# Kernel optimization log

Measured on AMD Instinct MI355X. Metric: run time of the kernel, lower is better.

The kernel has to match this reference:

```python
import jax, jax.numpy as jnp
import numpy as np

EMBED_DIM = 1024
NUM_HEADS = 16
HEAD_DIM = EMBED_DIM // NUM_HEADS
SCALING = HEAD_DIM ** -0.5
NEG_FILL = -1e30


def setup_inputs() -> dict:
    key = jax.random.key(0)
    k1, k2, k3 = jax.random.split(key, 3)
    T, B, E = 2048, 4, EMBED_DIM
    query = jax.random.normal(k1, (T, B, E), dtype=jnp.float32)
    key_padding_mask = jnp.zeros((B, T), dtype=bool)  # 1 = padded key
    # xavier_uniform-like init
    lim_in = (6.0 / (3 * E + E)) ** 0.5
    in_proj_weight = jax.random.uniform(k2, (3 * E, E), minval=-lim_in, maxval=lim_in, dtype=jnp.float32)
    in_proj_bias = jnp.zeros((3 * E,), dtype=jnp.float32)
    lim_out = (6.0 / (E + E)) ** 0.5
    out_w = jax.random.uniform(k3, (E, E), minval=-lim_out, maxval=lim_out, dtype=jnp.float32)
    out_b = jnp.zeros((E,), dtype=jnp.float32)
    return {"query": query, "key_padding_mask": key_padding_mask,
            "in_proj_weight": in_proj_weight, "in_proj_bias": in_proj_bias,
            "out_w": out_w, "out_b": out_b}


def reference(query, key_padding_mask, in_proj_weight, in_proj_bias, out_w, out_b):
    T, B, E = query.shape
    H, D = NUM_HEADS, HEAD_DIM
    # fused in-projection (self-attention: qkv from same input)
    qkv = query @ in_proj_weight.T + in_proj_bias  # [T,B,3E]
    q, k, v = jnp.split(qkv, 3, axis=-1)
    q = q * SCALING
    q = q.reshape(T, B, H, D)
    k = k.reshape(T, B, H, D)
    v = v.reshape(T, B, H, D)
    # attention scores [B,H,T,S]
    scores = jnp.einsum('tbhd,sbhd->bhts', q, k)
    scores = jnp.where(key_padding_mask[:, None, None, :], NEG_FILL, scores)
    attn_w = jax.nn.softmax(scores, axis=-1)  # [B,H,T,S]
    # weighted sum of values -> [T,B,E]
    attn = jnp.einsum('bhts,sbhd->tbhd', attn_w, v).reshape(T, B, E)
    attn = attn @ out_w.T + out_b
    attn_w_avg = jnp.sum(attn_w, axis=1) / H  # [B,T,S]
    return attn, attn_w_avg
```

## Files before the change

### kernel.cpp

```cpp
#include <hip/hip_runtime.h>
#include <stdint.h>

#define QSCALE 0.18033688011112042f

typedef unsigned short u16;
typedef unsigned int u32;
typedef __attribute__((ext_vector_type(8))) __bf16 bf16x8;
typedef __attribute__((ext_vector_type(4))) float f32x4;
typedef __attribute__((ext_vector_type(16))) float f32x16;
typedef __attribute__((ext_vector_type(8))) u16 u16x8;
typedef __attribute__((ext_vector_type(4))) u32 u32x4;

__device__ __forceinline__ void gl_lds16(const void* g, void* l) {
  __builtin_amdgcn_global_load_lds(
      (const __attribute__((address_space(1))) void*)g,
      (__attribute__((address_space(3))) void*)l, 16, 0, 0);
}

__device__ __forceinline__ u16 f2bf(float f) {
  unsigned int u = __float_as_uint(f);
  u += 0x7FFFu + ((u >> 16) & 1u);
  return (u16)(u >> 16);
}

extern "C" __global__ __launch_bounds__(256) void cvt_all(
    const float* __restrict__ query, const float* __restrict__ w_in,
    const float* __restrict__ w_out, u16* __restrict__ dst) {
  int i = (blockIdx.x * 256 + threadIdx.x) * 4;
  const float* src;
  int off;
  if (i < 8388608) {
    src = query; off = i;
  } else if (i < 11534336) {
    src = w_in; off = i - 8388608;
  } else {
    src = w_out; off = i - 11534336;
  }
  float4 v = *(const float4*)(src + off);
  ushort4 o;
  o.x = f2bf(v.x); o.y = f2bf(v.y); o.z = f2bf(v.z); o.w = f2bf(v.w);
  *(ushort4*)(dst + i) = o;
}

extern "C" __global__ __launch_bounds__(256) void gemm_qkv(
    const u16* __restrict__ X, const u16* __restrict__ W,
    const float* __restrict__ bias,
    u16* __restrict__ qb, u16* __restrict__ kb, u16* __restrict__ vb) {
  const int tid = threadIdx.x;
  const int w = tid >> 6, lane = tid & 63;
  const int lg = lane >> 4, ll = lane & 15;
  const int wm = w >> 1, wn = w & 1;
  const int row0A = blockIdx.x * 128;
  const int row0B = blockIdx.y * 128;

  __shared__ __align__(16) u16 As[2][128 * 32];
  __shared__ __align__(16) u16 Bs[2][128 * 32];

  f32x4 acc[4][4] = {};

  const int r_st = tid >> 2;
  const int cb_st = (tid & 3) * 16;

#pragma unroll
  for (int it = 0; it < 2; ++it) {
    gl_lds16((const char*)X + ((size_t)(row0A + it * 64 + r_st) * 1024) * 2 + cb_st,
             (char*)&As[0][0] + it * 4096 + w * 1024);
    gl_lds16((const char*)W + ((size_t)(row0B + it * 64 + r_st) * 1024) * 2 + cb_st,
             (char*)&Bs[0][0] + it * 4096 + w * 1024);
  }

  for (int kt = 0; kt < 32; ++kt) {
    const int cur = kt & 1;
    asm volatile("s_waitcnt vmcnt(0)" ::: "memory");
    __syncthreads();
    if (kt + 1 < 32) {
      const int k0 = (kt + 1) * 32;
#pragma unroll
      for (int it = 0; it < 2; ++it) {
        gl_lds16((const char*)X + ((size_t)(row0A + it * 64 + r_st) * 1024 + k0) * 2 + cb_st,
                 (char*)&As[cur ^ 1][0] + it * 4096 + w * 1024);
        gl_lds16((const char*)W + ((size_t)(row0B + it * 64 + r_st) * 1024 + k0) * 2 + cb_st,
                 (char*)&Bs[cur ^ 1][0] + it * 4096 + w * 1024);
      }
    }
    const u16* Ab = &As[cur][0];
    const u16* Bb = &Bs[cur][0];
    const int kc = lg * 8;
    bf16x8 a[4], bfr[4];
#pragma unroll
    for (int i = 0; i < 4; ++i)
      a[i] = *(const bf16x8*)(Ab + (wm * 64 + i * 16 + ll) * 32 + kc);
#pragma unroll
    for (int j = 0; j < 4; ++j)
      bfr[j] = *(const bf16x8*)(Bb + (wn * 64 + j * 16 + ll) * 32 + kc);
#pragma unroll
    for (int i = 0; i < 4; ++i)
#pragma unroll
      for (int j = 0; j < 4; ++j)
        acc[i][j] = __builtin_amdgcn_mfma_f32_16x16x32_bf16(a[i], bfr[j], acc[i][j], 0, 0, 0);
  }

  const int which = row0B >> 10;
  u16* dst = which == 0 ? qb : (which == 1 ? kb : vb);
  const float scl = which == 0 ? QSCALE : 1.0f;
#pragma unroll
  for (int j = 0; j < 4; ++j) {
    const int n = row0B + wn * 64 + j * 16 + ll;
    const float bv = bias[n];
    const int n2 = n & 1023;
    const int hh = n2 >> 6, dd = n2 & 63;
#pragma unroll
    for (int i = 0; i < 4; ++i)
#pragma unroll
      for (int r = 0; r < 4; ++r) {
        const int m = row0A + wm * 64 + i * 16 + lg * 4 + r;
        const int tt = m >> 2, bb = m & 3;
        dst[((size_t)(bb * 16 + hh) * 2048 + tt) * 64 + dd] = f2bf((acc[i][j][r] + bv) * scl);
      }
  }
}

extern "C" __global__ __launch_bounds__(256) void transpose_v(
    const u16* __restrict__ v, u16* __restrict__ vt) {
  const int blk = blockIdx.x;
  const int bh = blk >> 5, tt = blk & 31;
  const int t0 = tt * 64;
  const int tid = threadIdx.x;
  __shared__ __align__(16) u16 tile[64][72];
  const u16* src = v + ((size_t)bh * 2048 + t0) * 64;
#pragma unroll
  for (int it = 0; it < 2; ++it) {
    const int r = it * 32 + (tid >> 3);
    const int c = (tid & 7) * 8;
    *(u16x8*)(&tile[r][c]) = *(const u16x8*)(src + (size_t)r * 64 + c);
  }
  __syncthreads();
  u16* dstb = vt + (size_t)bh * 64 * 2048 + t0;
#pragma unroll
  for (int it = 0; it < 2; ++it) {
    const int d = it * 32 + (tid >> 3);
    const int s = (tid & 7) * 8;
    u16x8 o;
#pragma unroll
    for (int jj = 0; jj < 8; ++jj) o[jj] = tile[s + jj][d];
    *(u16x8*)(dstb + (size_t)d * 2048 + s) = o;
  }
}

extern "C" __global__ __launch_bounds__(256, 3) void flash_fwd(
    const u16* __restrict__ q, const u16* __restrict__ k,
    const u16* __restrict__ vt, const unsigned char* __restrict__ mask,
    u16* __restrict__ attn_pre, float* __restrict__ stat_il) {
  const int lb = ((blockIdx.x & 7) << 7) + (blockIdx.x >> 3);
  const int bh = lb >> 4, tt = lb & 15;
  const int b = bh >> 4, hd = bh & 15;
  const int t0 = tt * 128;
  const int tid = threadIdx.x, w = tid >> 6, lane = tid & 63;
  const int hl = lane >> 5;
  const int l31 = lane & 31;

  __shared__ __align__(16) u16 Ks[3][64 * 64];
  __shared__ __align__(16) u16 Vs[3][64 * 64];
  __shared__ __align__(16) unsigned char Ms[2048];

  const int qrow = t0 + w * 32 + l31;
  const u16* qp = q + ((size_t)bh * 2048 + qrow) * 64 + hl * 8;
  bf16x8 qreg[4];
#pragma unroll
  for (int kg = 0; kg < 4; ++kg) qreg[kg] = *(const bf16x8*)(qp + kg * 16);

  f32x16 po[2] = {};
  float lsum = 0.f;

  const int slot_r = tid >> 3;
  const int slot_c8 = (tid & 7) ^ (slot_r & 7);

#define STAGE3(buf, s0_)                                                       \
  do {                                                                         \
    _Pragma("unroll") for (int it2 = 0; it2 < 2; ++it2) {                      \
      const int rr = it2 * 32 + slot_r;                                        \
      gl_lds16((const char*)k +                                                \
                   (((size_t)bh * 2048 + (s0_) + rr) * 64 + slot_c8 * 8) * 2,  \
               (char*)&Ks[buf][0] + it2 * 4096 + w * 1024);                    \
      gl_lds16((const char*)vt +                                               \
                   (((size_t)bh * 64 + rr) * 2048 + (s0_) + slot_c8 * 8) * 2,  \
               (char*)&Vs[buf][0] + it2 * 4096 + w * 1024);                    \
    }                                                                          \
  } while (0)

  if (w < 2)
    gl_lds16((const char*)mask + b * 2048 + w * 1024 + lane * 16,
             (char*)Ms + w * 1024);
  STAGE3(0, 0);
  STAGE3(1, 64);

  for (int t = 0; t < 32; ++t) {
    if (t < 31) {
      asm volatile("s_waitcnt vmcnt(4)" ::: "memory");
    } else {
      asm volatile("s_waitcnt vmcnt(0)" ::: "memory");
    }
    __builtin_amdgcn_s_barrier();
    if (t + 2 < 32) STAGE3((t + 2) % 3, (t + 2) * 64);

    const int s0 = t * 64;
    const int cur = t % 3;
    const char* Kb = (const char*)&Ks[cur][0];
    const char* Vb = (const char*)&Vs[cur][0];

    u32 mq[8];
#pragma unroll
    for (int kt = 0; kt < 2; ++kt)
#pragma unroll
      for (int j = 0; j < 4; ++j)
        mq[kt * 4 + j] =
            *(const u32*)(Ms + s0 + kt * 32 + j * 8 + hl * 4);
    const u32 anym = mq[0] | mq[1] | mq[2] | mq[3] | mq[4] | mq[5] | mq[6] | mq[7];

#pragma unroll
    for (int kt = 0; kt < 2; ++kt) {
      f32x16 z = {};
      const int key = kt * 32 + l31;
#pragma unroll
      for (int kg = 0; kg < 4; ++kg) {
        const bf16x8 kf = *(const bf16x8*)(
            Kb + key * 128 + ((((kg << 1) | hl) ^ (key & 7)) << 4));
        z = __builtin_amdgcn_mfma_f32_32x32x16_bf16(kf, qreg[kg], z, 0, 0, 0);
      }

      float ps[16];
#pragma unroll
      for (int r = 0; r < 16; ++r) ps[r] = __builtin_amdgcn_exp2f(z[r]);
      if (__any(anym != 0)) {
#pragma unroll
        for (int r = 0; r < 16; ++r)
          if ((mq[kt * 4 + (r >> 2)] >> ((r & 3) * 8)) & 0xFFu) ps[r] = 0.f;
      }
#pragma unroll
      for (int r = 0; r < 16; ++r) lsum += ps[r];

      u32 w8[8];
#pragma unroll
      for (int j = 0; j < 4; ++j) {
        asm("v_cvt_pk_bf16_f32 %0, %1, %2"
            : "=v"(w8[2 * j]) : "v"(ps[4 * j]), "v"(ps[4 * j + 1]));
        asm("v_cvt_pk_bf16_f32 %0, %1, %2"
            : "=v"(w8[2 * j + 1]) : "v"(ps[4 * j + 2]), "v"(ps[4 * j + 3]));
      }

#pragma unroll
      for (int f = 0; f < 2; ++f) {
        u32 d0 = w8[4 * f], d1 = w8[4 * f + 1];
        u32 s0w = w8[4 * f + 2], s1w = w8[4 * f + 3];
        asm volatile("v_permlane32_swap_b32 %0, %1" : "+v"(d0), "+v"(s0w));
        asm volatile("v_permlane32_swap_b32 %0, %1" : "+v"(d1), "+v"(s1w));
        const bf16x8 pa = __builtin_bit_cast(bf16x8, (u32x4){d0, d1, s0w, s1w});
        const int g = kt * 2 + f;
#pragma unroll
        for (int dt = 0; dt < 2; ++dt) {
          const int d = dt * 32 + l31;
          const bf16x8 vf = *(const bf16x8*)(
              Vb + d * 128 + ((((g << 1) | hl) ^ (d & 7)) << 4));
          po[dt] = __builtin_amdgcn_mfma_f32_32x32x16_bf16(pa, vf, po[dt], 0, 0, 0);
        }
      }
    }
  }

  lsum += __shfl_xor(lsum, 32, 64);
  const float linv = 1.0f / lsum;
  if (lane < 32)
    stat_il[(size_t)bh * 2048 + t0 + w * 32 + lane] = linv;

#pragma unroll
  for (int r = 0; r < 16; ++r) {
    const int qi = (r & 3) + 8 * (r >> 2) + 4 * hl;
    const float lv = __shfl(linv, qi, 64);
    const int trow = t0 + w * 32 + qi;
#pragma unroll
    for (int dt = 0; dt < 2; ++dt) {
      const int dd = dt * 32 + l31;
      attn_pre[((size_t)(trow * 4 + b)) * 1024 + hd * 64 + dd] =
          f2bf(po[dt][r] * lv);
    }
  }
#undef STAGE3
}

extern "C" __global__ __launch_bounds__(256, 3) void wavg(
    const u16* __restrict__ q, const u16* __restrict__ k,
    const unsigned char* __restrict__ mask,
    const float* __restrict__ stat_il, float* __restrict__ wout) {
  const int lb = ((blockIdx.x & 7) << 8) + (blockIdx.x >> 3);
  const int b = lb >> 9, tt = (lb >> 5) & 15, st = lb & 31;
  const int t0 = tt * 128, s0 = st * 64;
  const int tid = threadIdx.x, w = tid >> 6, lane = tid & 63;
  const int hl = lane >> 5;
  const int l31 = lane & 31;

  __shared__ __align__(16) u16 Qs[2][128 * 64];
  __shared__ __align__(16) u16 Ks2[2][64 * 64];

  const int slot_r8 = tid >> 3;
  const int slot_c8 = (tid & 7) ^ (slot_r8 & 7);

  u32 mq[8];
#pragma unroll
  for (int kt = 0; kt < 2; ++kt)
#pragma unroll
    for (int j = 0; j < 4; ++j)
      mq[kt * 4 + j] = *(const u32*)(mask + b * 2048 + s0 + kt * 32 + j * 8 + hl * 4);
  const u32 anym = mq[0] | mq[1] | mq[2] | mq[3] | mq[4] | mq[5] | mq[6] | mq[7];
  const bool domask = __any(anym != 0);

#define STAGE_W(buf, hh)                                                       \
  do {                                                                         \
    const size_t qo_ = (size_t)(b * 16 + (hh)) * 2048;                         \
    _Pragma("unroll") for (int i2 = 0; i2 < 4; ++i2) {                         \
      const int rr = i2 * 32 + slot_r8;                                        \
      gl_lds16((const char*)q + ((qo_ + t0 + rr) * 64 + slot_c8 * 8) * 2,      \
               (char*)&Qs[buf][0] + i2 * 4096 + w * 1024);                     \
    }                                                                          \
    _Pragma("unroll") for (int i2 = 0; i2 < 2; ++i2) {                         \
      const int rr = i2 * 32 + slot_r8;                                        \
      gl_lds16((const char*)k + ((qo_ + s0 + rr) * 64 + slot_c8 * 8) * 2,      \
               (char*)&Ks2[buf][0] + i2 * 4096 + w * 1024);                    \
    }                                                                          \
  } while (0)

  STAGE_W(0, 0);
  asm volatile("s_waitcnt vmcnt(0)" ::: "memory");
  __syncthreads();

  float accw[32] = {};
  for (int h = 0; h < 16; ++h) {
    const int cur = h & 1;
    const float ilh =
        stat_il[(size_t)(b * 16 + h) * 2048 + t0 + w * 32 + l31];

    if (h + 1 < 16) STAGE_W(cur ^ 1, h + 1);

    const char* Qb = (const char*)&Qs[cur][0];
    const char* Kb = (const char*)&Ks2[cur][0];

    const int qr = w * 32 + l31;
    bf16x8 qf[4];
#pragma unroll
    for (int kg = 0; kg < 4; ++kg)
      qf[kg] = *(const bf16x8*)(
          Qb + qr * 128 + ((((kg << 1) | hl) ^ (qr & 7)) << 4));

#pragma unroll
    for (int kt = 0; kt < 2; ++kt) {
      f32x16 z = {};
      const int key = kt * 32 + l31;
#pragma unroll
      for (int kg = 0; kg < 4; ++kg) {
        const bf16x8 kf = *(const bf16x8*)(
            Kb + key * 128 + ((((kg << 1) | hl) ^ (key & 7)) << 4));
        z = __builtin_amdgcn_mfma_f32_32x32x16_bf16(kf, qf[kg], z, 0, 0, 0);
      }
      float ps[16];
#pragma unroll
      for (int r = 0; r < 16; ++r) ps[r] = __builtin_amdgcn_exp2f(z[r]);
      if (domask) {
#pragma unroll
        for (int r = 0; r < 16; ++r)
          if ((mq[kt * 4 + (r >> 2)] >> ((r & 3) * 8)) & 0xFFu) ps[r] = 0.f;
      }
#pragma unroll
      for (int r = 0; r < 16; ++r)
        accw[kt * 16 + r] = fmaf(ps[r], ilh, accw[kt * 16 + r]);
    }

    asm volatile("s_waitcnt vmcnt(0)" ::: "memory");
    __syncthreads();
  }

  float* tb = ((float*)&Qs[0][0]) + w * 2048;
#pragma unroll
  for (int kt = 0; kt < 2; ++kt)
#pragma unroll
    for (int j = 0; j < 4; ++j) {
      f32x4 qd;
#pragma unroll
      for (int e = 0; e < 4; ++e) qd[e] = accw[kt * 16 + 4 * j + e] * 0.0625f;
      const int slot = kt * 8 + 2 * j + hl;
      *(f32x4*)(tb + l31 * 64 + ((slot ^ (l31 & 7)) << 2)) = qd;
    }
  __syncthreads();
#pragma unroll
  for (int j2 = 0; j2 < 8; ++j2) {
    const int row = j2 * 4 + (lane >> 4);
    const int slot = lane & 15;
    const f32x4 v = *(const f32x4*)(tb + row * 64 + ((slot ^ (row & 7)) << 2));
    *(f32x4*)(wout + ((size_t)b * 2048 + t0 + w * 32 + row) * 2048 + s0 +
              slot * 4) = v;
  }
#undef STAGE_W
}

extern "C" __global__ __launch_bounds__(256) void gemm_out(
    const u16* __restrict__ A, const u16* __restrict__ W,
    const float* __restrict__ bias, float* __restrict__ out) {
  const int tid = threadIdx.x;
  const int w = tid >> 6, lane = tid & 63;
  const int lg = lane >> 4, ll = lane & 15;
  const int wm = w >> 1, wn = w & 1;
  const int row0A = blockIdx.x * 128;
  const int row0B = blockIdx.y * 128;

  __shared__ __align__(16) u16 As[2][128 * 32];
  __shared__ __align__(16) u16 Bs[2][128 * 32];

  f32x4 acc[4][4] = {};
  const int r_st = tid >> 2;
  const int cb_st = (tid & 3) * 16;

#pragma unroll
  for (int it = 0; it < 2; ++it) {
    gl_lds16((const char*)A + ((size_t)(row0A + it * 64 + r_st) * 1024) * 2 + cb_st,
             (char*)&As[0][0] + it * 4096 + w * 1024);
    gl_lds16((const char*)W + ((size_t)(row0B + it * 64 + r_st) * 1024) * 2 + cb_st,
             (char*)&Bs[0][0] + it * 4096 + w * 1024);
  }

  for (int kt = 0; kt < 32; ++kt) {
    const int cur = kt & 1;
    asm volatile("s_waitcnt vmcnt(0)" ::: "memory");
    __syncthreads();
    if (kt + 1 < 32) {
      const int k0 = (kt + 1) * 32;
#pragma unroll
      for (int it = 0; it < 2; ++it) {
        gl_lds16((const char*)A + ((size_t)(row0A + it * 64 + r_st) * 1024 + k0) * 2 + cb_st,
                 (char*)&As[cur ^ 1][0] + it * 4096 + w * 1024);
        gl_lds16((const char*)W + ((size_t)(row0B + it * 64 + r_st) * 1024 + k0) * 2 + cb_st,
                 (char*)&Bs[cur ^ 1][0] + it * 4096 + w * 1024);
      }
    }
    const u16* Ab = &As[cur][0];
    const u16* Bb = &Bs[cur][0];
    const int kc = lg * 8;
    bf16x8 a[4], bfr[4];
#pragma unroll
    for (int i = 0; i < 4; ++i)
      a[i] = *(const bf16x8*)(Ab + (wm * 64 + i * 16 + ll) * 32 + kc);
#pragma unroll
    for (int j = 0; j < 4; ++j)
      bfr[j] = *(const bf16x8*)(Bb + (wn * 64 + j * 16 + ll) * 32 + kc);
#pragma unroll
    for (int i = 0; i < 4; ++i)
#pragma unroll
      for (int j = 0; j < 4; ++j)
        acc[i][j] = __builtin_amdgcn_mfma_f32_16x16x32_bf16(a[i], bfr[j], acc[i][j], 0, 0, 0);
  }

#pragma unroll
  for (int j = 0; j < 4; ++j) {
    const int n = row0B + wn * 64 + j * 16 + ll;
    const float bv = bias[n];
#pragma unroll
    for (int i = 0; i < 4; ++i)
#pragma unroll
      for (int r = 0; r < 4; ++r) {
        const int m = row0A + wm * 64 + i * 16 + lg * 4 + r;
        out[(size_t)m * 1024 + n] = acc[i][j][r] + bv;
      }
  }
}

extern "C" void kernel_launch(void* const* d_in, const int* in_sizes, int n_in,
                              void* d_out, int out_size, void* d_ws, size_t ws_size,
                              hipStream_t stream) {
  const float* query = (const float*)d_in[0];
  const unsigned char* mask = (const unsigned char*)d_in[1];
  const float* w_in = (const float*)d_in[2];
  const float* b_in = (const float*)d_in[3];
  const float* w_out = (const float*)d_in[4];
  const float* b_out = (const float*)d_in[5];

  float* out0 = (float*)d_out;
  float* outw = out0 + (size_t)8388608;

  char* ws = (char*)d_ws;
  u16* Xbf   = (u16*)(ws + 0);
  u16* Wqkv  = (u16*)(ws + 16777216);
  u16* Woutb = (u16*)(ws + 23068672);
  u16* qb    = (u16*)(ws + 25165824);
  u16* kb    = (u16*)(ws + 41943040);
  u16* vb    = (u16*)(ws + 58720256);
  u16* vtb   = (u16*)(ws + 75497472);
  u16* ap    = (u16*)(ws + 92274688);
  float* sil = (float*)(ws + 109051904);

  cvt_all<<<12288, 256, 0, stream>>>(query, w_in, w_out, Xbf);
  gemm_qkv<<<dim3(64, 24), 256, 0, stream>>>(Xbf, Wqkv, b_in, qb, kb, vb);
  transpose_v<<<2048, 256, 0, stream>>>(vb, vtb);
  flash_fwd<<<1024, 256, 0, stream>>>(qb, kb, vtb, mask, ap, sil);
  wavg<<<2048, 256, 0, stream>>>(qb, kb, mask, sil, outw);
  gemm_out<<<dim3(64, 8), 256, 0, stream>>>(ap, Woutb, b_out, out0);
}
```

Measured before the change: 282.9 us.

## Software-pipeline QK and PV in flash kernel with bitpacked mask

New measurement: 289.9 us. +2.5%, slower.

```diff
diff --git a/kernel.cpp b/kernel.cpp
--- a/kernel.cpp
+++ b/kernel.cpp
@@ -5,6 +5,7 @@
 
 typedef unsigned short u16;
 typedef unsigned int u32;
+typedef unsigned long long u64;
 typedef __attribute__((ext_vector_type(8))) __bf16 bf16x8;
 typedef __attribute__((ext_vector_type(4))) float f32x4;
 typedef __attribute__((ext_vector_type(16))) float f32x16;
@@ -42,6 +43,21 @@
   *(ushort4*)(dst + i) = o;
 }
 
+extern "C" __global__ __launch_bounds__(128) void mask_bits(
+    const unsigned char* __restrict__ mask, u64* __restrict__ mbits) {
+  const int i = threadIdx.x;
+  const unsigned char* p = mask + i * 64;
+  u64 bits = 0;
+#pragma unroll
+  for (int j = 0; j < 8; ++j) {
+    const u64 c = *(const u64*)(p + j * 8);
+#pragma unroll
+    for (int bb = 0; bb < 8; ++bb)
+      if ((c >> (8 * bb)) & 0xFFull) bits |= 1ull << (j * 8 + bb);
+  }
+  mbits[i] = bits;
+}
+
 extern "C" __global__ __launch_bounds__(256) void gemm_qkv(
     const u16* __restrict__ X, const u16* __restrict__ W,
     const float* __restrict__ bias,
@@ -147,9 +163,9 @@
   }
 }
 
-extern "C" __global__ __launch_bounds__(256, 3) void flash_fwd(
+extern "C" __global__ __launch_bounds__(256, 4) void flash_fwd(
     const u16* __restrict__ q, const u16* __restrict__ k,
-    const u16* __restrict__ vt, const unsigned char* __restrict__ mask,
+    const u16* __restrict__ vt, const u64* __restrict__ mbits,
     u16* __restrict__ attn_pre, float* __restrict__ stat_il) {
   const int lb = ((blockIdx.x & 7) << 7) + (blockIdx.x >> 3);
   const int bh = lb >> 4, tt = lb & 15;
@@ -160,8 +176,7 @@
   const int l31 = lane & 31;
 
   __shared__ __align__(16) u16 Ks[3][64 * 64];
-  __shared__ __align__(16) u16 Vs[3][64 * 64];
-  __shared__ __align__(16) unsigned char Ms[2048];
+  __shared__ __align__(16) u16 Vs[2][64 * 64];
 
   const int qrow = t0 + w * 32 + l31;
   const u16* qp = q + ((size_t)bh * 2048 + qrow) * 64 + hl * 8;
@@ -175,96 +190,113 @@
   const int slot_r = tid >> 3;
   const int slot_c8 = (tid & 7) ^ (slot_r & 7);
 
-#define STAGE3(buf, s0_)                                                       \
+#define STAGE_K(s_, buf_)                                                      \
   do {                                                                         \
     _Pragma("unroll") for (int it2 = 0; it2 < 2; ++it2) {                      \
       const int rr = it2 * 32 + slot_r;                                        \
       gl_lds16((const char*)k +                                                \
-                   (((size_t)bh * 2048 + (s0_) + rr) * 64 + slot_c8 * 8) * 2,  \
-               (char*)&Ks[buf][0] + it2 * 4096 + w * 1024);                    \
-      gl_lds16((const char*)vt +                                               \
-                   (((size_t)bh * 64 + rr) * 2048 + (s0_) + slot_c8 * 8) * 2,  \
-               (char*)&Vs[buf][0] + it2 * 4096 + w * 1024);                    \
+                   (((size_t)bh * 2048 + (s_)*64 + rr) * 64 + slot_c8 * 8) * 2,\
+               (char*)&Ks[buf_][0] + it2 * 4096 + w * 1024);                   \
     }                                                                          \
   } while (0)
-
-  if (w < 2)
-    gl_lds16((const char*)mask + b * 2048 + w * 1024 + lane * 16,
-             (char*)Ms + w * 1024);
-  STAGE3(0, 0);
-  STAGE3(1, 64);
-
+#define STAGE_V(s_, buf_)                                                      \
+  do {                                                                         \
+    _Pragma("unroll") for (int it2 = 0; it2 < 2; ++it2) {                      \
+      const int rr = it2 * 32 + slot_r;                                        \
+      gl_lds16((const char*)vt +                                               \
+                   (((size_t)bh * 64 + rr) * 2048 + (s_)*64 + slot_c8 * 8) * 2,\
+               (char*)&Vs[buf_][0] + it2 * 4096 + w * 1024);                   \
+    }                                                                          \
+  } while (0)
+
+  auto QK = [&](int kbuf, int kt, f32x16& z) {
+    const char* Kb = (const char*)&Ks[kbuf][0];
+    f32x16 acc = {};
+    const int key = kt * 32 + l31;
+#pragma unroll
+    for (int kg = 0; kg < 4; ++kg) {
+      const bf16x8 kf = *(const bf16x8*)(
+          Kb + key * 128 + ((((kg << 1) | hl) ^ (key & 7)) << 4));
+      acc = __builtin_amdgcn_mfma_f32_32x32x16_bf16(kf, qreg[kg], acc, 0, 0, 0);
+    }
+    z = acc;
+  };
+
+  auto CONSUME = [&](int vbuf, int kt, const f32x16& z, u32 m32) {
+    u32 w8[8];
+#pragma unroll
+    for (int h2 = 0; h2 < 2; ++h2) {
+      float ps[8];
+#pragma unroll
+      for (int r = 0; r < 8; ++r) {
+        const int ri = h2 * 8 + r;
+        float p = __builtin_amdgcn_exp2f(z[ri]);
+        if (m32) {
+          const int bitpos = (ri & 3) + 8 * (ri >> 2) + 4 * hl;
+          if ((m32 >> bitpos) & 1u) p = 0.f;
+        }
+        lsum += p;
+        ps[r] = p;
+      }
+#pragma unroll
+      for (int j = 0; j < 2; ++j) {
+        asm("v_cvt_pk_bf16_f32 %0, %1, %2"
+            : "=v"(w8[h2 * 4 + 2 * j]) : "v"(ps[4 * j]), "v"(ps[4 * j + 1]));
+        asm("v_cvt_pk_bf16_f32 %0, %1, %2"
+            : "=v"(w8[h2 * 4 + 2 * j + 1]) : "v"(ps[4 * j + 2]), "v"(ps[4 * j + 3]));
+      }
+    }
+    const char* Vb = (const char*)&Vs[vbuf][0];
+#pragma unroll
+    for (int f = 0; f < 2; ++f) {
+      u32 d0 = w8[4 * f], d1 = w8[4 * f + 1];
+      u32 s0w = w8[4 * f + 2], s1w = w8[4 * f + 3];
+      asm volatile("v_permlane32_swap_b32 %0, %1" : "+v"(d0), "+v"(s0w));
+      asm volatile("v_permlane32_swap_b32 %0, %1" : "+v"(d1), "+v"(s1w));
+      const bf16x8 pa = __builtin_bit_cast(bf16x8, (u32x4){d0, d1, s0w, s1w});
+      const int g = kt * 2 + f;
+      __builtin_amdgcn_s_setprio(1);
+#pragma unroll
+      for (int dt = 0; dt < 2; ++dt) {
+        const int d = dt * 32 + l31;
+        const bf16x8 vf = *(const bf16x8*)(
+            Vb + d * 128 + ((((g << 1) | hl) ^ (d & 7)) << 4));
+        po[dt] = __builtin_amdgcn_mfma_f32_32x32x16_bf16(pa, vf, po[dt], 0, 0, 0);
+      }
+      __builtin_amdgcn_s_setprio(0);
+    }
+  };
+
+  STAGE_K(0, 0);
+  STAGE_K(1, 1);
+  STAGE_V(0, 0);
+  asm volatile("s_waitcnt vmcnt(0)" ::: "memory");
+  __builtin_amdgcn_s_barrier();
+
+  f32x16 zA, zB;
+  QK(0, 0, zA);
+
+  int kb0 = 0, kb1 = 1, kb2 = 2;
   for (int t = 0; t < 32; ++t) {
+    const u64 mb = mbits[b * 32 + t];
+    if (t + 2 < 32) STAGE_K(t + 2, kb2);
+    if (t + 1 < 32) STAGE_V(t + 1, (t + 1) & 1);
+
+    __builtin_amdgcn_s_setprio(1);
+    QK(kb0, 1, zB);
+    __builtin_amdgcn_s_setprio(0);
+    CONSUME(t & 1, 0, zA, (u32)mb);
+
     if (t < 31) {
-      asm volatile("s_waitcnt vmcnt(4)" ::: "memory");
-    } else {
-      asm volatile("s_waitcnt vmcnt(0)" ::: "memory");
-    }
+      __builtin_amdgcn_s_setprio(1);
+      QK(kb1, 0, zA);
+      __builtin_amdgcn_s_setprio(0);
+    }
+    CONSUME(t & 1, 1, zB, (u32)(mb >> 32));
+
+    asm volatile("s_waitcnt vmcnt(0)" ::: "memory");
     __builtin_amdgcn_s_barrier();
-    if (t + 2 < 32) STAGE3((t + 2) % 3, (t + 2) * 64);
-
-    const int s0 = t * 64;
-    const int cur = t % 3;
-    const char* Kb = (const char*)&Ks[cur][0];
-    const char* Vb = (const char*)&Vs[cur][0];
-
-    u32 mq[8];
-#pragma unroll
-    for (int kt = 0; kt < 2; ++kt)
-#pragma unroll
-      for (int j = 0; j < 4; ++j)
-        mq[kt * 4 + j] =
-            *(const u32*)(Ms + s0 + kt * 32 + j * 8 + hl * 4);
-    const u32 anym = mq[0] | mq[1] | mq[2] | mq[3] | mq[4] | mq[5] | mq[6] | mq[7];
-
-#pragma unroll
-    for (int kt = 0; kt < 2; ++kt) {
-      f32x16 z = {};
-      const int key = kt * 32 + l31;
-#pragma unroll
-      for (int kg = 0; kg < 4; ++kg) {
-        const bf16x8 kf = *(const bf16x8*)(
-            Kb + key * 128 + ((((kg << 1) | hl) ^ (key & 7)) << 4));
-        z = __builtin_amdgcn_mfma_f32_32x32x16_bf16(kf, qreg[kg], z, 0, 0, 0);
-      }
-
-      float ps[16];
-#pragma unroll
-      for (int r = 0; r < 16; ++r) ps[r] = __builtin_amdgcn_exp2f(z[r]);
-      if (__any(anym != 0)) {
-#pragma unroll
-        for (int r = 0; r < 16; ++r)
-          if ((mq[kt * 4 + (r >> 2)] >> ((r & 3) * 8)) & 0xFFu) ps[r] = 0.f;
-      }
-#pragma unroll
-      for (int r = 0; r < 16; ++r) lsum += ps[r];
-
-      u32 w8[8];
-#pragma unroll
-      for (int j = 0; j < 4; ++j) {
-        asm("v_cvt_pk_bf16_f32 %0, %1, %2"
-            : "=v"(w8[2 * j]) : "v"(ps[4 * j]), "v"(ps[4 * j + 1]));
-        asm("v_cvt_pk_bf16_f32 %0, %1, %2"
-            : "=v"(w8[2 * j + 1]) : "v"(ps[4 * j + 2]), "v"(ps[4 * j + 3]));
-      }
-
-#pragma unroll
-      for (int f = 0; f < 2; ++f) {
-        u32 d0 = w8[4 * f], d1 = w8[4 * f + 1];
-        u32 s0w = w8[4 * f + 2], s1w = w8[4 * f + 3];
-        asm volatile("v_permlane32_swap_b32 %0, %1" : "+v"(d0), "+v"(s0w));
-        asm volatile("v_permlane32_swap_b32 %0, %1" : "+v"(d1), "+v"(s1w));
-        const bf16x8 pa = __builtin_bit_cast(bf16x8, (u32x4){d0, d1, s0w, s1w});
-        const int g = kt * 2 + f;
-#pragma unroll
-        for (int dt = 0; dt < 2; ++dt) {
-          const int d = dt * 32 + l31;
-          const bf16x8 vf = *(const bf16x8*)(
-              Vb + d * 128 + ((((g << 1) | hl) ^ (d & 7)) << 4));
-          po[dt] = __builtin_amdgcn_mfma_f32_32x32x16_bf16(pa, vf, po[dt], 0, 0, 0);
-        }
-      }
-    }
+    const int tmp = kb0; kb0 = kb1; kb1 = kb2; kb2 = tmp;
   }
 
   lsum += __shfl_xor(lsum, 32, 64);
@@ -284,12 +316,13 @@
           f2bf(po[dt][r] * lv);
     }
   }
-#undef STAGE3
+#undef STAGE_K
+#undef STAGE_V
 }
 
 extern "C" __global__ __launch_bounds__(256, 3) void wavg(
     const u16* __restrict__ q, const u16* __restrict__ k,
-    const unsigned char* __restrict__ mask,
+    const u64* __restrict__ mbits,
     const float* __restrict__ stat_il, float* __restrict__ wout) {
   const int lb = ((blockIdx.x & 7) << 8) + (blockIdx.x >> 3);
   const int b = lb >> 9, tt = (lb >> 5) & 15, st = lb & 31;
@@ -304,14 +337,9 @@
   const int slot_r8 = tid >> 3;
   const int slot_c8 = (tid & 7) ^ (slot_r8 & 7);
 
-  u32 mq[8];
-#pragma unroll
-  for (int kt = 0; kt < 2; ++kt)
-#pragma unroll
-    for (int j = 0; j < 4; ++j)
-      mq[kt * 4 + j] = *(const u32*)(mask + b * 2048 + s0 + kt * 32 + j * 8 + hl * 4);
-  const u32 anym = mq[0] | mq[1] | mq[2] | mq[3] | mq[4] | mq[5] | mq[6] | mq[7];
-  const bool domask = __any(anym != 0);
+  const u64 mbw = mbits[b * 32 + st];
+  const u32 m32lo = (u32)mbw, m32hi = (u32)(mbw >> 32);
+  const bool domask = mbw != 0ull;
 
 #define STAGE_W(buf, hh)                                                       \
   do {                                                                         \
@@ -350,27 +378,41 @@
       qf[kg] = *(const bf16x8*)(
           Qb + qr * 128 + ((((kg << 1) | hl) ^ (qr & 7)) << 4));
 
-#pragma unroll
-    for (int kt = 0; kt < 2; ++kt) {
-      f32x16 z = {};
-      const int key = kt * 32 + l31;
-#pragma unroll
-      for (int kg = 0; kg < 4; ++kg) {
-        const bf16x8 kf = *(const bf16x8*)(
-            Kb + key * 128 + ((((kg << 1) | hl) ^ (key & 7)) << 4));
-        z = __builtin_amdgcn_mfma_f32_32x32x16_bf16(kf, qf[kg], z, 0, 0, 0);
-      }
-      float ps[16];
-#pragma unroll
-      for (int r = 0; r < 16; ++r) ps[r] = __builtin_amdgcn_exp2f(z[r]);
+    f32x16 z0 = {}, z1 = {};
+    __builtin_amdgcn_s_setprio(1);
+#pragma unroll
+    for (int kg = 0; kg < 4; ++kg) {
+      const int key = l31;
+      const bf16x8 kf = *(const bf16x8*)(
+          Kb + key * 128 + ((((kg << 1) | hl) ^ (key & 7)) << 4));
+      z0 = __builtin_amdgcn_mfma_f32_32x32x16_bf16(kf, qf[kg], z0, 0, 0, 0);
+    }
+#pragma unroll
+    for (int kg = 0; kg < 4; ++kg) {
+      const int key = 32 + l31;
+      const bf16x8 kf = *(const bf16x8*)(
+          Kb + key * 128 + ((((kg << 1) | hl) ^ (key & 7)) << 4));
+      z1 = __builtin_amdgcn_mfma_f32_32x32x16_bf16(kf, qf[kg], z1, 0, 0, 0);
+    }
+    __builtin_amdgcn_s_setprio(0);
+
+#pragma unroll
+    for (int r = 0; r < 16; ++r) {
+      float p = __builtin_amdgcn_exp2f(z0[r]);
       if (domask) {
-#pragma unroll
-        for (int r = 0; r < 16; ++r)
-          if ((mq[kt * 4 + (r >> 2)] >> ((r & 3) * 8)) & 0xFFu) ps[r] = 0.f;
-      }
-#pragma unroll
-      for (int r = 0; r < 16; ++r)
-        accw[kt * 16 + r] = fmaf(ps[r], ilh, accw[kt * 16 + r]);
+        const int bitpos = (r & 3) + 8 * (r >> 2) + 4 * hl;
+        if ((m32lo >> bitpos) & 1u) p = 0.f;
+      }
+      accw[r] = fmaf(p, ilh, accw[r]);
+    }
+#pragma unroll
+    for (int r = 0; r < 16; ++r) {
+      float p = __builtin_amdgcn_exp2f(z1[r]);
+      if (domask) {
+        const int bitpos = (r & 3) + 8 * (r >> 2) + 4 * hl;
+        if ((m32hi >> bitpos) & 1u) p = 0.f;
+      }
+      accw[16 + r] = fmaf(p, ilh, accw[16 + r]);
     }
 
     asm volatile("s_waitcnt vmcnt(0)" ::: "memory");
@@ -493,11 +535,13 @@
   u16* vtb   = (u16*)(ws + 75497472);
   u16* ap    = (u16*)(ws + 92274688);
   float* sil = (float*)(ws + 109051904);
+  u64* mbits = (u64*)(ws + 109576192);
 
   cvt_all<<<12288, 256, 0, stream>>>(query, w_in, w_out, Xbf);
+  mask_bits<<<1, 128, 0, stream>>>(mask, mbits);
   gemm_qkv<<<dim3(64, 24), 256, 0, stream>>>(Xbf, Wqkv, b_in, qb, kb, vb);
   transpose_v<<<2048, 256, 0, stream>>>(vb, vtb);
-  flash_fwd<<<1024, 256, 0, stream>>>(qb, kb, vtb, mask, ap, sil);
-  wavg<<<2048, 256, 0, stream>>>(qb, kb, mask, sil, outw);
+  flash_fwd<<<1024, 256, 0, stream>>>(qb, kb, vtb, mbits, ap, sil);
+  wavg<<<2048, 256, 0, stream>>>(qb, kb, mbits, sil, outw);
   gemm_out<<<dim3(64, 8), 256, 0, stream>>>(ap, Woutb, b_out, out0);
 }
```
